# Optimization experiments

Measured on AMD Instinct MI355X. Metric: run time of the kernel, lower is better.

## Reference

```python
import jax, jax.numpy as jnp
import numpy as np

N_HEADS = 16
DIM = 1024
NEG_INF = -1e20  # neginf for fp32 per original module


def setup_inputs() -> dict:
    key = jax.random.key(0)
    ks = jax.random.split(key, 10)
    B, N, D = 2, 2048, DIM
    std = np.sqrt(2.0 / (D + D))  # xavier_normal for square weights
    inp = {
        "query": jax.random.normal(ks[0], (B, N, D), dtype=jnp.float32),
        "mask": jax.random.randint(ks[1], (B, N), 0, 2, dtype=jnp.int32),
        "wq": jax.random.normal(ks[2], (D, D), dtype=jnp.float32) * std,
        "bq": jnp.zeros((D,), dtype=jnp.float32),
        "wk": jax.random.normal(ks[3], (D, D), dtype=jnp.float32) * std,
        "bk": jnp.zeros((D,), dtype=jnp.float32),
        "wv": jax.random.normal(ks[4], (D, D), dtype=jnp.float32) * std,
        "bv": jnp.zeros((D,), dtype=jnp.float32),
        "wo": jax.random.normal(ks[5], (D, D), dtype=jnp.float32) * std,
        "bo": jnp.zeros((D,), dtype=jnp.float32),
    }
    return inp


def reference(query, mask, wq, bq, wk, bk, wv, bv, wo, bo):
    B, N, D = query.shape
    H = N_HEADS
    dh = D // H
    scale = jnp.asarray(np.sqrt(dh), dtype=query.dtype)

    def heads(x):  # [B,N,D] -> [B,H,N,dh]
        return x.reshape(B, N, H, dh).transpose(0, 2, 1, 3)

    q = heads(query @ wq.T + bq) / scale
    k = heads(query @ wk.T + bk)
    v = heads(query @ wv.T + bv)

    # [B,H,Nq,Nk] scaled dot-product scores, masked where mask==0
    dot_prod = jnp.einsum("bhqd,bhkd->bhqk", q, k)
    dot_prod = jnp.where(mask[:, None, None, :] == 0, NEG_INF, dot_prod)

    attn = jax.nn.softmax(dot_prod.astype(jnp.float32), axis=-1).astype(query.dtype)
    # dropout p=0 -> identity
    ctx = jnp.einsum("bhqk,bhkd->bhqd", attn, v)
    ctx = ctx.transpose(0, 2, 1, 3).reshape(B, N, D)
    out = ctx @ wo.T + bo
    # original returns dot_prod as [B*H, Nq, Nk]
    return out, dot_prod.reshape(B * H, N, N)
```

## Files before the change

### kernel.cpp

```cpp
#include <hip/hip_runtime.h>

typedef unsigned short u16;
typedef unsigned int u32;
typedef __attribute__((ext_vector_type(8))) __bf16 bf16x8;
typedef __attribute__((ext_vector_type(4))) float f32x4;

#define MFMA(a, b, c) __builtin_amdgcn_mfma_f32_16x16x32_bf16((a), (b), (c), 0, 0, 0)

__device__ __forceinline__ u16 f2bf(float f) {
  union { float f; unsigned u; } v; v.f = f;
  unsigned r = v.u + 0x7fffu + ((v.u >> 16) & 1u);
  return (u16)(r >> 16);
}

__device__ __forceinline__ void gld16(const u16* g, u16* l) {
  __builtin_amdgcn_global_load_lds(
      (const __attribute__((address_space(1))) unsigned int*)(g),
      (__attribute__((address_space(3))) unsigned int*)(l), 16, 0, 0);
}

__global__ __launch_bounds__(256) void k_cast(
    const float* __restrict__ query, const float* __restrict__ wq,
    const float* __restrict__ wk, const float* __restrict__ wv,
    const float* __restrict__ wo, u16* __restrict__ dst)
{
  size_t i = ((size_t)blockIdx.x * 256 + threadIdx.x) * 8;
  const float* src; size_t off; float sc = 1.0f;
  if (i < 4194304u)      { src = query; off = i; }
  else if (i < 5242880u) { src = wq; off = i - 4194304u; sc = 0.125f; }
  else if (i < 6291456u) { src = wk; off = i - 5242880u; }
  else if (i < 7340032u) { src = wv; off = i - 6291456u; }
  else                   { src = wo; off = i - 7340032u; }
  float4 a = *(const float4*)(src + off);
  float4 b = *(const float4*)(src + off + 4);
  alignas(16) u16 r[8] = { f2bf(a.x*sc), f2bf(a.y*sc), f2bf(a.z*sc), f2bf(a.w*sc),
                           f2bf(b.x*sc), f2bf(b.y*sc), f2bf(b.z*sc), f2bf(b.w*sc) };
  *(int4*)(dst + i) = *(int4*)r;
}

__global__ __launch_bounds__(256) void k_gemm_qkv(
    const u16* __restrict__ Ab, const u16* __restrict__ Wb,
    const float* __restrict__ bq, const float* __restrict__ bk, const float* __restrict__ bv,
    u16* __restrict__ Qh, u16* __restrict__ Kh, u16* __restrict__ Vt)
{
  const int fb = blockIdx.x;
  const int sb = (fb & 7) * 96 + (fb >> 3);
  const int n0 = (sb % 24) * 128;
  const int m0 = (sb / 24) * 128;
  const int tid = threadIdx.x;
  const int w = tid >> 6, lane = tid & 63, g = lane >> 4, l15 = lane & 15;
  const int wm = w >> 1, wn = w & 1;
  __shared__ alignas(16) u16 As[128 * 32];
  __shared__ alignas(16) u16 Bs[128 * 32];
  f32x4 acc[4][4] = {};
  for (int k0 = 0; k0 < 1024; k0 += 32) {
    __syncthreads();
#pragma unroll
    for (int t = 0; t < 2; ++t) {
      int i = t * 256 + tid;
      int row = i >> 2, ch = i & 3, sch = ch ^ (row & 3);
      gld16(Ab + (size_t)(m0 + row) * 1024 + k0 + sch * 8, As + i * 8);
    }
#pragma unroll
    for (int t = 0; t < 2; ++t) {
      int i = t * 256 + tid;
      int row = i >> 2, ch = i & 3, sch = ch ^ (row & 3);
      gld16(Wb + (size_t)(n0 + row) * 1024 + k0 + sch * 8, Bs + i * 8);
    }
    __syncthreads();
    bf16x8 af[4], bfr[4];
#pragma unroll
    for (int i = 0; i < 4; ++i) {
      int row = wm * 64 + i * 16 + l15;
      af[i] = *(const bf16x8*)(As + (row * 4 + (g ^ (row & 3))) * 8);
    }
#pragma unroll
    for (int j = 0; j < 4; ++j) {
      int row = wn * 64 + j * 16 + l15;
      bfr[j] = *(const bf16x8*)(Bs + (row * 4 + (g ^ (row & 3))) * 8);
    }
#pragma unroll
    for (int i = 0; i < 4; ++i)
#pragma unroll
      for (int j = 0; j < 4; ++j)
        acc[i][j] = MFMA(af[i], bfr[j], acc[i][j]);
  }
  const int proj = n0 >> 10;
  const float* bias = (proj == 0) ? bq : (proj == 1) ? bk : bv;
  const float bsc = (proj == 0) ? 0.125f : 1.0f;
#pragma unroll
  for (int i = 0; i < 4; ++i)
#pragma unroll
    for (int j = 0; j < 4; ++j)
#pragma unroll
      for (int jj = 0; jj < 4; ++jj) {
        int mr = m0 + wm * 64 + i * 16 + g * 4 + jj;
        int c  = n0 + wn * 64 + j * 16 + l15;
        int d = c & 1023, h = d >> 6, d64 = d & 63;
        int b = mr >> 11, n = mr & 2047;
        int bh = (b << 4) | h;
        float v = acc[i][j][jj] + bias[d] * bsc;
        if (proj == 2) {
          Vt[((size_t)bh * 64 + d64) * 2048 + n] = f2bf(v);
        } else {
          u16* dst = (proj == 0) ? Qh : Kh;
          dst[((size_t)bh * 2048 + n) * 64 + d64] = f2bf(v);
        }
      }
}

__global__ __launch_bounds__(256) void k_gemm_out(
    const u16* __restrict__ Ab, const u16* __restrict__ Wb,
    const float* __restrict__ bo, float* __restrict__ out)
{
  const int fb = blockIdx.x;
  const int sb = (fb & 7) * 32 + (fb >> 3);
  const int n0 = (sb & 7) * 128;
  const int m0 = (sb >> 3) * 128;
  const int tid = threadIdx.x;
  const int w = tid >> 6, lane = tid & 63, g = lane >> 4, l15 = lane & 15;
  const int wm = w >> 1, wn = w & 1;
  __shared__ alignas(16) u16 As[128 * 32];
  __shared__ alignas(16) u16 Bs[128 * 32];
  f32x4 acc[4][4] = {};
  for (int k0 = 0; k0 < 1024; k0 += 32) {
    __syncthreads();
#pragma unroll
    for (int t = 0; t < 2; ++t) {
      int i = t * 256 + tid;
      int row = i >> 2, ch = i & 3, sch = ch ^ (row & 3);
      gld16(Ab + (size_t)(m0 + row) * 1024 + k0 + sch * 8, As + i * 8);
    }
#pragma unroll
    for (int t = 0; t < 2; ++t) {
      int i = t * 256 + tid;
      int row = i >> 2, ch = i & 3, sch = ch ^ (row & 3);
      gld16(Wb + (size_t)(n0 + row) * 1024 + k0 + sch * 8, Bs + i * 8);
    }
    __syncthreads();
    bf16x8 af[4], bfr[4];
#pragma unroll
    for (int i = 0; i < 4; ++i) {
      int row = wm * 64 + i * 16 + l15;
      af[i] = *(const bf16x8*)(As + (row * 4 + (g ^ (row & 3))) * 8);
    }
#pragma unroll
    for (int j = 0; j < 4; ++j) {
      int row = wn * 64 + j * 16 + l15;
      bfr[j] = *(const bf16x8*)(Bs + (row * 4 + (g ^ (row & 3))) * 8);
    }
#pragma unroll
    for (int i = 0; i < 4; ++i)
#pragma unroll
      for (int j = 0; j < 4; ++j)
        acc[i][j] = MFMA(af[i], bfr[j], acc[i][j]);
  }
#pragma unroll
  for (int i = 0; i < 4; ++i)
#pragma unroll
    for (int j = 0; j < 4; ++j)
#pragma unroll
      for (int jj = 0; jj < 4; ++jj) {
        int mr = m0 + wm * 64 + i * 16 + g * 4 + jj;
        int c  = n0 + wn * 64 + j * 16 + l15;
        out[(size_t)mr * 1024 + c] = acc[i][j][jj] + bo[c];
      }
}

__global__ __launch_bounds__(256) void k_attn(
    const u16* __restrict__ Qh, const u16* __restrict__ Kh, const u16* __restrict__ Vt,
    const int* __restrict__ mask, float* __restrict__ dout, u16* __restrict__ ctx)
{
  const int fb = blockIdx.x;
  const int sb = (fb & 7) * 128 + (fb >> 3);
  const int qt = sb & 31;
  const int bh = sb >> 5;
  const int b  = bh >> 4;
  const int tid = threadIdx.x;
  const int w = tid >> 6, lane = tid & 63, g = lane >> 4, l15 = lane & 15;
  __shared__ alignas(16) u16 Ks[128 * 64];
  __shared__ alignas(16) u16 Vs[64 * 128];
  __shared__ alignas(16) u16 Ps[4][16 * 140];

  const u16* Qrow = Qh + ((size_t)bh * 2048 + qt * 64 + w * 16 + l15) * 64;
  bf16x8 qf0 = *(const bf16x8*)(Qrow + g * 8);
  bf16x8 qf1 = *(const bf16x8*)(Qrow + 32 + g * 8);

  float m[4] = {-3e38f, -3e38f, -3e38f, -3e38f};
  float l[4] = {0.f, 0.f, 0.f, 0.f};
  f32x4 O[4] = {};
  const int* maskb = mask + b * 2048;
  float* Sbase = dout + 4194304 + (size_t)bh * 4194304
               + (size_t)(qt * 64 + w * 16 + g * 4) * 2048 + l15;

  for (int kt = 0; kt < 16; ++kt) {
    __syncthreads();
    const u16* Kg = Kh + ((size_t)bh * 2048 + kt * 128) * 64;
#pragma unroll
    for (int it = 0; it < 4; ++it) {
      int i = it * 256 + tid;
      int row = i >> 3, ch = i & 7, sch = ch ^ (row & 7);
      gld16(Kg + row * 64 + sch * 8, Ks + i * 8);
    }
    const u16* Vg = Vt + (size_t)bh * 131072 + kt * 128;
#pragma unroll
    for (int it = 0; it < 4; ++it) {
      int i = it * 256 + tid;
      int row = i >> 4, ch = i & 15, sch = ch ^ (row & 15);
      gld16(Vg + (size_t)row * 2048 + sch * 8, Vs + i * 8);
    }
    int mk[8];
#pragma unroll
    for (int f = 0; f < 8; ++f) mk[f] = maskb[kt * 128 + f * 16 + l15];
    __syncthreads();

    f32x4 s[8];
#pragma unroll
    for (int f = 0; f < 8; ++f) {
      int row = f * 16 + l15;
      bf16x8 kf0 = *(const bf16x8*)(Ks + (row * 8 + ((0 + g) ^ (row & 7))) * 8);
      bf16x8 kf1 = *(const bf16x8*)(Ks + (row * 8 + ((4 + g) ^ (row & 7))) * 8);
      f32x4 t = {};
      t = MFMA(qf0, kf0, t);
      t = MFMA(qf1, kf1, t);
      s[f] = t;
    }

    float fb8[8];
#pragma unroll
    for (int f = 0; f < 8; ++f) fb8[f] = (mk[f] != 0) ? 0.f : -1e20f;

    float mloc[4] = {-3e38f, -3e38f, -3e38f, -3e38f};
#pragma unroll
    for (int jj = 0; jj < 4; ++jj)
#pragma unroll
      for (int f = 0; f < 8; ++f) {
        float sv = s[f][jj] + fb8[f];
        s[f][jj] = sv;
        Sbase[(size_t)jj * 2048 + kt * 128 + f * 16] = sv;
        mloc[jj] = fmaxf(mloc[jj], sv);
      }
#pragma unroll
    for (int d = 1; d < 16; d <<= 1)
#pragma unroll
      for (int jj = 0; jj < 4; ++jj)
        mloc[jj] = fmaxf(mloc[jj], __shfl_xor(mloc[jj], d, 64));

    float corr[4];
#pragma unroll
    for (int jj = 0; jj < 4; ++jj) {
      float mn = fmaxf(m[jj], mloc[jj]);
      corr[jj] = __expf(m[jj] - mn);
      m[jj] = mn;
    }
    float psum[4] = {0.f, 0.f, 0.f, 0.f};
#pragma unroll
    for (int f = 0; f < 8; ++f)
#pragma unroll
      for (int jj = 0; jj < 4; ++jj) {
        float p = __expf(s[f][jj] - m[jj]);
        psum[jj] += p;
        Ps[w][(g * 4 + jj) * 140 + f * 16 + l15] = f2bf(p);
      }
#pragma unroll
    for (int d = 1; d < 16; d <<= 1)
#pragma unroll
      for (int jj = 0; jj < 4; ++jj)
        psum[jj] += __shfl_xor(psum[jj], d, 64);
#pragma unroll
    for (int jj = 0; jj < 4; ++jj) l[jj] = l[jj] * corr[jj] + psum[jj];
#pragma unroll
    for (int fd = 0; fd < 4; ++fd)
#pragma unroll
      for (int jj = 0; jj < 4; ++jj) O[fd][jj] *= corr[jj];

#pragma unroll
    for (int fk = 0; fk < 4; ++fk) {
      bf16x8 pa = *(const bf16x8*)(&Ps[w][l15 * 140 + fk * 32 + g * 8]);
#pragma unroll
      for (int fd = 0; fd < 4; ++fd) {
        int row = fd * 16 + l15;
        bf16x8 bv = *(const bf16x8*)(Vs + (row * 16 + ((fk * 4 + g) ^ (row & 15))) * 8);
        O[fd] = MFMA(pa, bv, O[fd]);
      }
    }
  }
  float inv[4];
#pragma unroll
  for (int jj = 0; jj < 4; ++jj) inv[jj] = 1.0f / l[jj];
  const int h = bh & 15;
#pragma unroll
  for (int fd = 0; fd < 4; ++fd)
#pragma unroll
    for (int jj = 0; jj < 4; ++jj) {
      int n = qt * 64 + w * 16 + g * 4 + jj;
      int c = h * 64 + fd * 16 + l15;
      ctx[((size_t)(b * 2048 + n)) * 1024 + c] = f2bf(O[fd][jj] * inv[jj]);
    }
}

extern "C" void kernel_launch(void* const* d_in, const int* in_sizes, int n_in,
                              void* d_out, int out_size, void* d_ws, size_t ws_size,
                              hipStream_t stream)
{
  const float* query = (const float*)d_in[0];
  const int*   mask  = (const int*)d_in[1];
  const float* wq = (const float*)d_in[2];
  const float* bq = (const float*)d_in[3];
  const float* wk = (const float*)d_in[4];
  const float* bk = (const float*)d_in[5];
  const float* wv = (const float*)d_in[6];
  const float* bv = (const float*)d_in[7];
  const float* wo = (const float*)d_in[8];
  const float* bo = (const float*)d_in[9];
  float* out = (float*)d_out;

  u16* ws   = (u16*)d_ws;
  u16* Ab   = ws;
  u16* Wqkv = ws + 4194304;
  u16* Wo   = ws + 7340032;
  u16* Qh   = ws + 8388608;
  u16* Kh   = ws + 12582912;
  u16* Vt   = ws + 16777216;
  u16* ctx  = ws + 20971520;

  k_cast<<<4096, 256, 0, stream>>>(query, wq, wk, wv, wo, ws);
  k_gemm_qkv<<<768, 256, 0, stream>>>(Ab, Wqkv, bq, bk, bv, Qh, Kh, Vt);
  k_attn<<<1024, 256, 0, stream>>>(Qh, Kh, Vt, mask, out, ctx);
  k_gemm_out<<<256, 256, 0, stream>>>(ctx, Wo, bo, out);
}
```

Baseline: 250.5 us.

## Double-buffer K/V tiles with 64-key steps and nontemporal score stores

Splits the attention key loop into 64-key tiles and double-buffers the K and V shared-memory tiles. The next tile is prefetched asynchronously with global_load_lds while the current one is computed, replacing the synchronous load-then-compute loop. Score stores to the large dot_prod output become nontemporal to cut cache pollution. Costs are twice as many loop iterations, more barriers and online-softmax rescales, and reliance on a hand-written vmcnt(16) that must match the count of outstanding memory ops, including the mask loads and score stores.

```diff
diff --git a/kernel.cpp b/kernel.cpp
--- a/kernel.cpp
+++ b/kernel.cpp
@@ -178,13 +178,38 @@
   const int b  = bh >> 4;
   const int tid = threadIdx.x;
   const int w = tid >> 6, lane = tid & 63, g = lane >> 4, l15 = lane & 15;
-  __shared__ alignas(16) u16 Ks[128 * 64];
-  __shared__ alignas(16) u16 Vs[64 * 128];
-  __shared__ alignas(16) u16 Ps[4][16 * 140];
+  __shared__ alignas(16) u16 Ks[2][64 * 64];
+  __shared__ alignas(16) u16 Vs[2][64 * 64];
+  __shared__ alignas(16) u16 Ps[4][16 * 72];
 
   const u16* Qrow = Qh + ((size_t)bh * 2048 + qt * 64 + w * 16 + l15) * 64;
   bf16x8 qf0 = *(const bf16x8*)(Qrow + g * 8);
   bf16x8 qf1 = *(const bf16x8*)(Qrow + 32 + g * 8);
+
+  const u16* Kb = Kh + (size_t)bh * 131072;
+  const u16* Vb = Vt + (size_t)bh * 131072;
+
+  auto stageK = [&](int buf, int kt) {
+#pragma unroll
+    for (int it = 0; it < 2; ++it) {
+      int i = it * 256 + tid;
+      int row = i >> 3, ch = i & 7, sch = ch ^ (row & 7);
+      gld16(Kb + (size_t)(kt * 64 + row) * 64 + sch * 8, &Ks[buf][i * 8]);
+    }
+  };
+  auto stageV = [&](int buf, int kt) {
+#pragma unroll
+    for (int it = 0; it < 2; ++it) {
+      int i = it * 256 + tid;
+      int row = i >> 3, ch = i & 7, sch = ch ^ (row & 7);
+      gld16(Vb + (size_t)row * 2048 + kt * 64 + sch * 8, &Vs[buf][i * 8]);
+    }
+  };
+
+  stageK(0, 0); stageV(0, 0);
+  asm volatile("s_waitcnt vmcnt(0)" ::: "memory");
+  __builtin_amdgcn_s_barrier();
+  __builtin_amdgcn_sched_barrier(0);
 
   float m[4] = {-3e38f, -3e38f, -3e38f, -3e38f};
   float l[4] = {0.f, 0.f, 0.f, 0.f};
@@ -193,51 +218,43 @@
   float* Sbase = dout + 4194304 + (size_t)bh * 4194304
                + (size_t)(qt * 64 + w * 16 + g * 4) * 2048 + l15;
 
-  for (int kt = 0; kt < 16; ++kt) {
-    __syncthreads();
-    const u16* Kg = Kh + ((size_t)bh * 2048 + kt * 128) * 64;
-#pragma unroll
-    for (int it = 0; it < 4; ++it) {
-      int i = it * 256 + tid;
-      int row = i >> 3, ch = i & 7, sch = ch ^ (row & 7);
-      gld16(Kg + row * 64 + sch * 8, Ks + i * 8);
-    }
-    const u16* Vg = Vt + (size_t)bh * 131072 + kt * 128;
-#pragma unroll
-    for (int it = 0; it < 4; ++it) {
-      int i = it * 256 + tid;
-      int row = i >> 4, ch = i & 15, sch = ch ^ (row & 15);
-      gld16(Vg + (size_t)row * 2048 + sch * 8, Vs + i * 8);
-    }
-    int mk[8];
-#pragma unroll
-    for (int f = 0; f < 8; ++f) mk[f] = maskb[kt * 128 + f * 16 + l15];
-    __syncthreads();
-
-    f32x4 s[8];
-#pragma unroll
-    for (int f = 0; f < 8; ++f) {
+  int cur = 0;
+  for (int kt = 0; kt < 32; ++kt) {
+    asm volatile("s_waitcnt vmcnt(16)" ::: "memory");
+    __builtin_amdgcn_s_barrier();
+    __builtin_amdgcn_sched_barrier(0);
+
+    if (kt + 1 < 32) { stageK(cur ^ 1, kt + 1); stageV(cur ^ 1, kt + 1); }
+    __builtin_amdgcn_sched_barrier(0);
+
+    int mk[4];
+#pragma unroll
+    for (int f = 0; f < 4; ++f) mk[f] = maskb[kt * 64 + f * 16 + l15];
+
+    f32x4 s[4];
+#pragma unroll
+    for (int f = 0; f < 4; ++f) {
       int row = f * 16 + l15;
-      bf16x8 kf0 = *(const bf16x8*)(Ks + (row * 8 + ((0 + g) ^ (row & 7))) * 8);
-      bf16x8 kf1 = *(const bf16x8*)(Ks + (row * 8 + ((4 + g) ^ (row & 7))) * 8);
+      bf16x8 kf0 = *(const bf16x8*)(&Ks[cur][(row * 8 + ((0 + g) ^ (row & 7))) * 8]);
+      bf16x8 kf1 = *(const bf16x8*)(&Ks[cur][(row * 8 + ((4 + g) ^ (row & 7))) * 8]);
       f32x4 t = {};
       t = MFMA(qf0, kf0, t);
       t = MFMA(qf1, kf1, t);
       s[f] = t;
     }
 
-    float fb8[8];
-#pragma unroll
-    for (int f = 0; f < 8; ++f) fb8[f] = (mk[f] != 0) ? 0.f : -1e20f;
+    float fb4[4];
+#pragma unroll
+    for (int f = 0; f < 4; ++f) fb4[f] = (mk[f] != 0) ? 0.f : -1e20f;
 
     float mloc[4] = {-3e38f, -3e38f, -3e38f, -3e38f};
 #pragma unroll
     for (int jj = 0; jj < 4; ++jj)
 #pragma unroll
-      for (int f = 0; f < 8; ++f) {
-        float sv = s[f][jj] + fb8[f];
+      for (int f = 0; f < 4; ++f) {
+        float sv = s[f][jj] + fb4[f];
         s[f][jj] = sv;
-        Sbase[(size_t)jj * 2048 + kt * 128 + f * 16] = sv;
+        __builtin_nontemporal_store(sv, &Sbase[(size_t)jj * 2048 + kt * 64 + f * 16]);
         mloc[jj] = fmaxf(mloc[jj], sv);
       }
 #pragma unroll
@@ -255,12 +272,12 @@
     }
     float psum[4] = {0.f, 0.f, 0.f, 0.f};
 #pragma unroll
-    for (int f = 0; f < 8; ++f)
+    for (int f = 0; f < 4; ++f)
 #pragma unroll
       for (int jj = 0; jj < 4; ++jj) {
         float p = __expf(s[f][jj] - m[jj]);
         psum[jj] += p;
-        Ps[w][(g * 4 + jj) * 140 + f * 16 + l15] = f2bf(p);
+        Ps[w][(g * 4 + jj) * 72 + f * 16 + l15] = f2bf(p);
       }
 #pragma unroll
     for (int d = 1; d < 16; d <<= 1)
@@ -275,15 +292,16 @@
       for (int jj = 0; jj < 4; ++jj) O[fd][jj] *= corr[jj];
 
 #pragma unroll
-    for (int fk = 0; fk < 4; ++fk) {
-      bf16x8 pa = *(const bf16x8*)(&Ps[w][l15 * 140 + fk * 32 + g * 8]);
+    for (int fk = 0; fk < 2; ++fk) {
+      bf16x8 pa = *(const bf16x8*)(&Ps[w][l15 * 72 + fk * 32 + g * 8]);
 #pragma unroll
       for (int fd = 0; fd < 4; ++fd) {
         int row = fd * 16 + l15;
-        bf16x8 bv = *(const bf16x8*)(Vs + (row * 16 + ((fk * 4 + g) ^ (row & 15))) * 8);
+        bf16x8 bv = *(const bf16x8*)(&Vs[cur][(row * 8 + ((fk * 4 + g) ^ (row & 7))) * 8]);
         O[fd] = MFMA(pa, bv, O[fd]);
       }
     }
+    cur ^= 1;
   }
   float inv[4];
 #pragma unroll
```

New measurement: 220.3 us. 12.1% less time.
